# Performance work log

Measured on AMD Instinct MI355X. Metric: run time of the kernel, lower is better.

Reference implementation:

```python
import jax, jax.numpy as jnp
import numpy as np

B, T, DIM = 2, 2048, 2048
N_HEADS, N_KV_HEADS = 32, 8
HEAD_DIM = DIM // N_HEADS          # 64
N_REP = N_HEADS // N_KV_HEADS      # 4
ROPE_THETA = 10000.0


def setup_inputs() -> dict:
    key = jax.random.key(0)
    ks = jax.random.split(key, 5)
    x = jax.random.normal(ks[0], (B, T, DIM), dtype=jnp.float32)
    # RoPE frequencies: freqs_cis[t, j] = exp(i * t * theta^{-2j/head_dim})
    inv_freq = 1.0 / (ROPE_THETA ** (jnp.arange(0, HEAD_DIM, 2, dtype=jnp.float32) / HEAD_DIM))
    angles = jnp.arange(T, dtype=jnp.float32)[:, None] * inv_freq[None, :]  # [T, HEAD_DIM//2]
    cos, sin = jnp.cos(angles), jnp.sin(angles)
    s = 0.02
    wq = jax.random.normal(ks[1], (N_HEADS * HEAD_DIM, DIM), dtype=jnp.float32) * s
    wk = jax.random.normal(ks[2], (N_KV_HEADS * HEAD_DIM, DIM), dtype=jnp.float32) * s
    wv = jax.random.normal(ks[3], (N_KV_HEADS * HEAD_DIM, DIM), dtype=jnp.float32) * s
    wo = jax.random.normal(ks[4], (DIM, DIM), dtype=jnp.float32) * s
    return {"x": x, "cos": cos, "sin": sin, "wq": wq, "wk": wk, "wv": wv, "wo": wo}


def _apply_rope(t, cos, sin):
    # t: [B, T, H, D]; cos/sin: [T, D//2]. Complex multiply on interleaved pairs.
    b, tt, h, d = t.shape
    tr = t.reshape(b, tt, h, d // 2, 2)
    t0, t1 = tr[..., 0], tr[..., 1]
    c = cos[None, :, None, :]
    s = sin[None, :, None, :]
    o0 = t0 * c - t1 * s
    o1 = t0 * s + t1 * c
    return jnp.stack([o0, o1], axis=-1).reshape(b, tt, h, d)


def reference(x, cos, sin, wq, wk, wv, wo):
    Bs, Ts, C = x.shape
    # Projections (nn.Linear, no bias): y = x @ W^T
    q = jnp.einsum('btc,oc->bto', x, wq).reshape(Bs, Ts, N_HEADS, HEAD_DIM)
    k = jnp.einsum('btc,oc->bto', x, wk).reshape(Bs, Ts, N_KV_HEADS, HEAD_DIM)
    v = jnp.einsum('btc,oc->bto', x, wv).reshape(Bs, Ts, N_KV_HEADS, HEAD_DIM)
    q = _apply_rope(q, cos[:Ts], sin[:Ts])
    k = _apply_rope(k, cos[:Ts], sin[:Ts])
    # [B, H, T, D]; GQA: broadcast kv heads via grouped einsum instead of repeat.
    q = q.transpose(0, 2, 1, 3).reshape(Bs, N_KV_HEADS, N_REP, Ts, HEAD_DIM)
    k = k.transpose(0, 2, 1, 3)  # [B, Hkv, T, D]
    v = v.transpose(0, 2, 1, 3)
    scale = 1.0 / jnp.sqrt(jnp.asarray(HEAD_DIM, dtype=x.dtype))
    scores = jnp.einsum('bgrqd,bgkd->bgrqk', q, k) * scale  # [B, Hkv, rep, T, T]
    causal = jnp.tril(jnp.ones((Ts, Ts), dtype=bool))
    scores = jnp.where(causal, scores, jnp.finfo(scores.dtype).min)
    attn = jax.nn.softmax(scores, axis=-1)
    y = jnp.einsum('bgrqk,bgkd->bgrqd', attn, v)           # [B, Hkv, rep, T, D]
    y = y.reshape(Bs, N_HEADS, Ts, HEAD_DIM).transpose(0, 2, 1, 3).reshape(Bs, Ts, C)
    return jnp.einsum('btc,oc->bto', y, wo)
```

## Files before the change

kernel.cpp:

```cpp
#include <hip/hip_runtime.h>

typedef __bf16 bf16;
typedef __attribute__((ext_vector_type(8))) __bf16 bf16x8;
typedef __attribute__((ext_vector_type(4))) __bf16 bf16x4;
typedef __attribute__((ext_vector_type(4))) float f32x4;

constexpr int T_SEQ = 2048;
constexpr int DIM   = 2048;
constexpr int NH    = 32;
constexpr int NKV   = 8;
constexpr int HD    = 64;
constexpr int QKV_N = DIM + 2 * NKV * HD;
constexpr int MROWS = 2 * T_SEQ;

__global__ void cast_all_kernel(const float* __restrict__ x,
                                const float* __restrict__ wq, const float* __restrict__ wk,
                                const float* __restrict__ wv, const float* __restrict__ wo,
                                bf16* __restrict__ xb, bf16* __restrict__ wqkv,
                                bf16* __restrict__ wob) {
  int stride = gridDim.x * blockDim.x;
  for (int g = blockIdx.x * blockDim.x + threadIdx.x; g < 4718592; g += stride) {
    const float* src; bf16* dst; int off;
    if (g < 2097152)      { src = x;  dst = xb;             off = g; }
    else if (g < 3145728) { src = wq; dst = wqkv;           off = g - 2097152; }
    else if (g < 3407872) { src = wk; dst = wqkv + 4194304; off = g - 3145728; }
    else if (g < 3670016) { src = wv; dst = wqkv + 5242880; off = g - 3407872; }
    else                  { src = wo; dst = wob;            off = g - 3670016; }
    float4 v = *(const float4*)(src + (size_t)off * 4);
    bf16x4 o = { (bf16)v.x, (bf16)v.y, (bf16)v.z, (bf16)v.w };
    *(bf16x4*)(dst + (size_t)off * 4) = o;
  }
}

__device__ inline void rect_decode(int orig, int& bmi, int& bni) {
  int c = orig & 7, i = orig >> 3;
  bmi = (c & 1) * 8 + (i & 7);
  bni = (c >> 1) * 4 + (i >> 3);
}

__global__ __launch_bounds__(512) void gemm256(const bf16* __restrict__ A,
                                               const bf16* __restrict__ W,
                                               float* __restrict__ C,
                                               int N, int K) {
  constexpr int BM = 256, BN = 128, BK = 64;
  __shared__ __attribute__((aligned(16))) bf16 Ab[3][BM * BK];
  __shared__ __attribute__((aligned(16))) bf16 Bb[3][BN * BK];
  const int tid = threadIdx.x, lane = tid & 63, wave = tid >> 6;
  const int l15 = lane & 15, l4 = lane >> 4;
  int bmi, bni;
  rect_decode(blockIdx.x, bmi, bni);
  const int bm = bmi * BM, bn = bni * BN;
  const int wm = (wave >> 1) * 64, wn = (wave & 1) * 64;

  f32x4 acc[4][4] = {};

  const int NT = K / BK;
  auto stage = [&](int s, int k0) {
    #pragma unroll
    for (int i = 0; i < 4; ++i) {
      int c = i * 512 + tid;
      int row = c >> 3;
      int gc = ((c & 7) ^ (row & 7)) << 3;
      __builtin_amdgcn_global_load_lds(
          (const __attribute__((address_space(1))) unsigned int*)(A + (size_t)(bm + row) * K + k0 + gc),
          (__attribute__((address_space(3))) unsigned int*)(&Ab[s][0] + c * 8), 16, 0, 0);
    }
    #pragma unroll
    for (int i = 0; i < 2; ++i) {
      int c = i * 512 + tid;
      int row = c >> 3;
      int gc = ((c & 7) ^ (row & 7)) << 3;
      __builtin_amdgcn_global_load_lds(
          (const __attribute__((address_space(1))) unsigned int*)(W + (size_t)(bn + row) * K + k0 + gc),
          (__attribute__((address_space(3))) unsigned int*)(&Bb[s][0] + c * 8), 16, 0, 0);
    }
  };

  stage(0, 0);
  stage(1, BK);

  int d = 0;
  for (int t = 0; t < NT; ++t) {
    if (t + 1 < NT) { asm volatile("s_waitcnt vmcnt(6)" ::: "memory"); }
    else            { asm volatile("s_waitcnt vmcnt(0)" ::: "memory"); }
    __builtin_amdgcn_s_barrier();

    bf16x8 af[2][4], bfr[2][4];
    #pragma unroll
    for (int kk = 0; kk < 2; ++kk) {
      #pragma unroll
      for (int mi = 0; mi < 4; ++mi) {
        int row = wm + mi * 16 + l15;
        af[kk][mi] = *(const bf16x8*)((const char*)&Ab[d][0] + row * 128 +
                                      (((kk * 4 + l4) ^ (row & 7)) << 4));
      }
      #pragma unroll
      for (int ni = 0; ni < 4; ++ni) {
        int row = wn + ni * 16 + l15;
        bfr[kk][ni] = *(const bf16x8*)((const char*)&Bb[d][0] + row * 128 +
                                       (((kk * 4 + l4) ^ (row & 7)) << 4));
      }
    }

    if (t + 2 < NT) {
      int s = d + 2; if (s >= 3) s -= 3;
      stage(s, (t + 2) * BK);
    }

    __builtin_amdgcn_s_setprio(1);
    #pragma unroll
    for (int kk = 0; kk < 2; ++kk)
      #pragma unroll
      for (int mi = 0; mi < 4; ++mi)
        #pragma unroll
        for (int ni = 0; ni < 4; ++ni)
          acc[mi][ni] = __builtin_amdgcn_mfma_f32_16x16x32_bf16(af[kk][mi], bfr[kk][ni],
                                                                acc[mi][ni], 0, 0, 0);
    __builtin_amdgcn_s_setprio(0);

    ++d; if (d == 3) d = 0;
  }

  #pragma unroll
  for (int mi = 0; mi < 4; ++mi)
    #pragma unroll
    for (int ni = 0; ni < 4; ++ni) {
      size_t row = (size_t)bm + wm + mi * 16 + l4 * 4;
      int col = bn + wn + ni * 16 + l15;
      #pragma unroll
      for (int r = 0; r < 4; ++r)
        C[(row + r) * N + col] = acc[mi][ni][r];
    }
}

__global__ __launch_bounds__(512, 1) void gemm192(const bf16* __restrict__ A,
                                                  const bf16* __restrict__ W,
                                                  bf16* __restrict__ C,
                                                  const float* __restrict__ cs,
                                                  const float* __restrict__ sn) {
  constexpr int BM = 256, BN = 192, BK = 64, N = QKV_N, K = DIM;
  __shared__ __attribute__((aligned(16))) bf16 Ab[3][BM * BK];
  __shared__ __attribute__((aligned(16))) bf16 Bb[2][BN * BK];
  const int tid = threadIdx.x, lane = tid & 63, wave = tid >> 6;
  const int l15 = lane & 15, l4 = lane >> 4;
  int bmi, bni;
  rect_decode(blockIdx.x, bmi, bni);
  const int bm = bmi * BM, bn = bni * BN;
  const int wm = (wave >> 1) * 64, wn = (wave & 1) * 96;

  f32x4 acc[4][6] = {};

  constexpr int NT = K / BK;
  auto stageA = [&](int s, int k0) {
    #pragma unroll
    for (int i = 0; i < 4; ++i) {
      int c = i * 512 + tid;
      int row = c >> 3;
      int gc = ((c & 7) ^ (row & 7)) << 3;
      __builtin_amdgcn_global_load_lds(
          (const __attribute__((address_space(1))) unsigned int*)(A + (size_t)(bm + row) * K + k0 + gc),
          (__attribute__((address_space(3))) unsigned int*)(&Ab[s][0] + c * 8), 16, 0, 0);
    }
  };
  auto stageB = [&](int s, int k0) {
    #pragma unroll
    for (int i = 0; i < 3; ++i) {
      int c = i * 512 + tid;
      int row = c >> 3;
      int gc = ((c & 7) ^ (row & 7)) << 3;
      __builtin_amdgcn_global_load_lds(
          (const __attribute__((address_space(1))) unsigned int*)(W + (size_t)(bn + row) * K + k0 + gc),
          (__attribute__((address_space(3))) unsigned int*)(&Bb[s][0] + c * 8), 16, 0, 0);
    }
  };

  stageA(0, 0);
  stageB(0, 0);
  stageA(1, BK);

  for (int t = 0; t < NT; ++t) {
    const int d3 = t % 3, db = t & 1;
    if (t + 1 < NT) { asm volatile("s_waitcnt vmcnt(4)" ::: "memory"); }
    else            { asm volatile("s_waitcnt vmcnt(0)" ::: "memory"); }
    __builtin_amdgcn_s_barrier();

    bf16x8 af[2][4], bfr[2][6];
    #pragma unroll
    for (int kk = 0; kk < 2; ++kk) {
      #pragma unroll
      for (int mi = 0; mi < 4; ++mi) {
        int row = wm + mi * 16 + l15;
        af[kk][mi] = *(const bf16x8*)((const char*)&Ab[d3][0] + row * 128 +
                                      (((kk * 4 + l4) ^ (row & 7)) << 4));
      }
      #pragma unroll
      for (int ni = 0; ni < 6; ++ni) {
        int row = wn + ni * 16 + l15;
        bfr[kk][ni] = *(const bf16x8*)((const char*)&Bb[db][0] + row * 128 +
                                       (((kk * 4 + l4) ^ (row & 7)) << 4));
      }
    }

    if (t + 1 < NT) stageB(db ^ 1, (t + 1) * BK);
    if (t + 2 < NT) { int s = d3 + 2; if (s >= 3) s -= 3; stageA(s, (t + 2) * BK); }

    __builtin_amdgcn_s_setprio(1);
    #pragma unroll
    for (int kk = 0; kk < 2; ++kk)
      #pragma unroll
      for (int mi = 0; mi < 4; ++mi)
        #pragma unroll
        for (int ni = 0; ni < 6; ++ni)
          acc[mi][ni] = __builtin_amdgcn_mfma_f32_16x16x32_bf16(af[kk][mi], bfr[kk][ni],
                                                                acc[mi][ni], 0, 0, 0);
    __builtin_amdgcn_s_setprio(0);
  }

  const bool odd = (l15 & 1);
  #pragma unroll
  for (int ni = 0; ni < 6; ++ni) {
    if (bn + wn + ni * 16 < 2560) {
      int col = bn + wn + ni * 16 + l15;
      int ip = (col & 63) >> 1;
      #pragma unroll
      for (int mi = 0; mi < 4; ++mi) {
        int row0 = wm + mi * 16 + l4 * 4;
        #pragma unroll
        for (int r = 0; r < 4; ++r) {
          int tpos = (bm + row0 + r) & (T_SEQ - 1);
          float c = cs[tpos * 32 + ip];
          float s = sn[tpos * 32 + ip];
          float a = acc[mi][ni][r];
          float p = __shfl_xor(a, 1);
          acc[mi][ni][r] = odd ? (p * s + a * c) : (a * c - p * s);
        }
      }
    }
  }

  #pragma unroll
  for (int mi = 0; mi < 4; ++mi)
    #pragma unroll
    for (int ni = 0; ni < 6; ++ni) {
      size_t row = (size_t)bm + wm + mi * 16 + l4 * 4;
      int col = bn + wn + ni * 16 + l15;
      #pragma unroll
      for (int r = 0; r < 4; ++r)
        C[(row + r) * N + col] = (bf16)acc[mi][ni][r];
    }
}

__global__ __launch_bounds__(512, 2) void attn_kernel(const bf16* __restrict__ qkv,
                                                      bf16* __restrict__ y) {
  const int h = blockIdx.x, b = blockIdx.z;
  const int strip = 15 - blockIdx.y;
  const int g = h >> 2;
  const int tid = threadIdx.x, lane = tid & 63, wave = tid >> 6;
  const int l15 = lane & 15, l4 = lane >> 4;
  const int qbase = strip * 128 + wave * 16;

  __shared__ __attribute__((aligned(16))) bf16 Kb[2][128 * 64];
  __shared__ __attribute__((aligned(16))) bf16 VTs[2][2][64 * 64];
  __shared__ __attribute__((aligned(16))) bf16 Pb[8][16 * 64];

  constexpr float SCALE2 = 0.125f * 1.44269504088896f;
  constexpr float THR_RAW = 8.0f / SCALE2;
  constexpr int VOFF = DIM + NKV * HD;

  const bf16 one1 = (bf16)1.0f;
  const bf16x8 ones = { one1, one1, one1, one1, one1, one1, one1, one1 };

  bf16x8 qf[2];
  {
    const bf16* qp = qkv + ((size_t)b * T_SEQ + qbase + l15) * QKV_N + h * HD + l4 * 8;
    qf[0] = *(const bf16x8*)(qp);
    qf[1] = *(const bf16x8*)(qp + 32);
  }

  f32x4 oacc[4] = {};
  f32x4 lacc = {};
  float m_run = -INFINITY;
  const int qg = qbase + l15;

  const int nt = strip + 1;
  const size_t kvbase = (size_t)b * T_SEQ;
  const int vwoff = ((lane * 128 + wave * 16) ^ ((lane & 7) << 4));

  {
    #pragma unroll
    for (int i = 0; i < 2; ++i) {
      int chunk = i * 512 + tid;
      int row = chunk >> 3;
      int csrc = ((chunk & 7) << 3) ^ ((row & 7) << 3);
      __builtin_amdgcn_global_load_lds(
          (const __attribute__((address_space(1))) unsigned int*)
              (qkv + (kvbase + row) * QKV_N + DIM + g * HD + csrc),
          (__attribute__((address_space(3))) unsigned int*)(&Kb[0][0] + chunk * 8), 16, 0, 0);
    }
    #pragma unroll
    for (int hf = 0; hf < 2; ++hf) {
      const bf16* vp = qkv + (kvbase + hf * 64 + wave * 8) * QKV_N + VOFF + g * HD + lane;
      bf16x8 vr;
      #pragma unroll
      for (int j = 0; j < 8; ++j) vr[j] = vp[(size_t)j * QKV_N];
      *(bf16x8*)((char*)&VTs[0][hf][0] + vwoff) = vr;
    }
    asm volatile("s_waitcnt vmcnt(0)" ::: "memory");
    __syncthreads();
  }

  int cur = 0;
  for (int kt = 0; kt < nt; ++kt) {
    const bool has_next = (kt + 1) < nt;
    bf16x8 vr0, vr1;
    if (has_next) {
      #pragma unroll
      for (int i = 0; i < 2; ++i) {
        int chunk = i * 512 + tid;
        int row = chunk >> 3;
        int csrc = ((chunk & 7) << 3) ^ ((row & 7) << 3);
        __builtin_amdgcn_global_load_lds(
            (const __attribute__((address_space(1))) unsigned int*)
                (qkv + (kvbase + (kt + 1) * 128 + row) * QKV_N + DIM + g * HD + csrc),
            (__attribute__((address_space(3))) unsigned int*)(&Kb[cur ^ 1][0] + chunk * 8), 16, 0, 0);
      }
      const bf16* vp0 = qkv + (kvbase + (kt + 1) * 128 + wave * 8) * QKV_N + VOFF + g * HD + lane;
      const bf16* vp1 = vp0 + (size_t)64 * QKV_N;
      #pragma unroll
      for (int j = 0; j < 8; ++j) vr0[j] = vp0[(size_t)j * QKV_N];
      #pragma unroll
      for (int j = 0; j < 8; ++j) vr1[j] = vp1[(size_t)j * QKV_N];
    }

    const bf16* kb = &Kb[cur][0];
    const bool diag = (kt == strip);

    #pragma unroll
    for (int hf = 0; hf < 2; ++hf) {
      if (diag && hf == 1 && wave < 4) continue;

      f32x4 z[4];
      #pragma unroll
      for (int nt4 = 0; nt4 < 4; ++nt4) z[nt4] = (f32x4){0.f, 0.f, 0.f, 0.f};
      #pragma unroll
      for (int nt4 = 0; nt4 < 4; ++nt4)
        #pragma unroll
        for (int kk = 0; kk < 2; ++kk) {
          bf16x8 kf = *(const bf16x8*)((const char*)kb +
              (((hf * 64 + nt4 * 16 + l15) * 128 + (kk * 32 + l4 * 8) * 2) ^ ((l15 & 7) << 4)));
          z[nt4] = __builtin_amdgcn_mfma_f32_16x16x32_bf16(kf, qf[kk], z[nt4], 0, 0, 0);
        }

      if (diag) {
        #pragma unroll
        for (int nt4 = 0; nt4 < 4; ++nt4)
          #pragma unroll
          for (int r = 0; r < 4; ++r)
            if (kt * 128 + hf * 64 + nt4 * 16 + l4 * 4 + r > qg) z[nt4][r] = -INFINITY;
      }

      float a0 = fmaxf(fmaxf(z[0][0], z[0][1]), z[0][2]);
      float a1 = fmaxf(fmaxf(z[0][3], z[1][0]), z[1][1]);
      float a2 = fmaxf(fmaxf(z[1][2], z[1][3]), z[2][0]);
      float a3 = fmaxf(fmaxf(z[2][1], z[2][2]), z[2][3]);
      float a4 = fmaxf(fmaxf(z[3][0], z[3][1]), z[3][2]);
      float b0 = fmaxf(fmaxf(a0, a1), a2);
      float b1 = fmaxf(fmaxf(a3, a4), z[3][3]);
      float vm = fmaxf(b0, b1);
      vm = fmaxf(vm, __shfl_xor(vm, 16));
      vm = fmaxf(vm, __shfl_xor(vm, 32));

      if (!__all(vm - m_run <= THR_RAW)) {
        float mnew = fmaxf(m_run, vm);
        float alpha = __builtin_amdgcn_exp2f((m_run - mnew) * SCALE2);
        #pragma unroll
        for (int r = 0; r < 4; ++r) lacc[r] *= alpha;
        #pragma unroll
        for (int dt = 0; dt < 4; ++dt)
          #pragma unroll
          for (int r = 0; r < 4; ++r) oacc[dt][r] *= alpha;
        m_run = mnew;
      }
      const float ms = m_run * SCALE2;

      #pragma unroll
      for (int nt4 = 0; nt4 < 4; ++nt4)
        #pragma unroll
        for (int r = 0; r < 4; ++r)
          z[nt4][r] = __builtin_amdgcn_exp2f(__builtin_fmaf(z[nt4][r], SCALE2, -ms));

      bf16* pbw = &Pb[wave][0];
      #pragma unroll
      for (int nt4 = 0; nt4 < 4; ++nt4) {
        bf16x4 pk = { (bf16)z[nt4][0], (bf16)z[nt4][1], (bf16)z[nt4][2], (bf16)z[nt4][3] };
        *(bf16x4*)((char*)pbw + ((l15 * 128 + nt4 * 32 + l4 * 8) ^ ((l15 & 7) << 4))) = pk;
      }

      const bf16* vt = &VTs[cur][hf][0];
      #pragma unroll
      for (int kk = 0; kk < 2; ++kk) {
        bf16x8 pf = *(const bf16x8*)((const char*)pbw +
            ((l15 * 128 + kk * 64 + l4 * 16) ^ ((l15 & 7) << 4)));
        lacc = __builtin_amdgcn_mfma_f32_16x16x32_bf16(ones, pf, lacc, 0, 0, 0);
        #pragma unroll
        for (int dt = 0; dt < 4; ++dt) {
          bf16x8 vf = *(const bf16x8*)((const char*)vt +
              (((dt * 16 + l15) * 128 + (kk * 32 + l4 * 8) * 2) ^ ((l15 & 7) << 4)));
          oacc[dt] = __builtin_amdgcn_mfma_f32_16x16x32_bf16(vf, pf, oacc[dt], 0, 0, 0);
        }
      }
    }

    if (has_next) {
      *(bf16x8*)((char*)&VTs[cur ^ 1][0][0] + vwoff) = vr0;
      *(bf16x8*)((char*)&VTs[cur ^ 1][1][0] + vwoff) = vr1;
      __syncthreads();
      cur ^= 1;
    }
  }

  {
    float linv = __builtin_amdgcn_rcpf(lacc[0]);
    bf16* yp = y + ((size_t)b * T_SEQ + qbase + l15) * DIM + h * HD + l4 * 4;
    #pragma unroll
    for (int dt = 0; dt < 4; ++dt) {
      bf16x4 ov = { (bf16)(oacc[dt][0] * linv), (bf16)(oacc[dt][1] * linv),
                    (bf16)(oacc[dt][2] * linv), (bf16)(oacc[dt][3] * linv) };
      *(bf16x4*)(yp + dt * 16) = ov;
    }
  }
}

extern "C" void kernel_launch(void* const* d_in, const int* in_sizes, int n_in,
                              void* d_out, int out_size, void* d_ws, size_t ws_size,
                              hipStream_t stream) {
  const float* x    = (const float*)d_in[0];
  const float* cosb = (const float*)d_in[1];
  const float* sinb = (const float*)d_in[2];
  const float* wq   = (const float*)d_in[3];
  const float* wk   = (const float*)d_in[4];
  const float* wv   = (const float*)d_in[5];
  const float* wo   = (const float*)d_in[6];
  float* out = (float*)d_out;

  bf16* xb   = (bf16*)d_ws;
  bf16* wqkv = xb + (size_t)MROWS * DIM;
  bf16* wob  = wqkv + (size_t)QKV_N * DIM;
  bf16* qkv  = wob + (size_t)DIM * DIM;
  bf16* y    = qkv + (size_t)MROWS * QKV_N;

  cast_all_kernel<<<2048, 256, 0, stream>>>(x, wq, wk, wv, wo, xb, wqkv, wob);

  gemm192<<<256, 512, 0, stream>>>(xb, wqkv, qkv, cosb, sinb);

  attn_kernel<<<dim3(NH, 16, 2), 512, 0, stream>>>(qkv, y);

  gemm256<<<256, 512, 0, stream>>>(y, wob, out, DIM, DIM);
}
```

Baseline: 164.4 us.

## Process two 256-row query strips per attention block with paired causal balancing

The attention kernel now gives each wave 32 query rows (two 16-row fragments), so every K/V fragment loaded from LDS feeds two MFMAs. Each block handles a long strip (7-p) and a short strip p back-to-back to balance causal work, which shrinks the grid from 1024 to 256 blocks. Launch bounds drop to one block per SM to make room for the doubled accumulators and P buffer. The risks are lower occupancy, fewer blocks than a full wave across the CUs, and some tiles where only part of the waves have causal work to do.

```diff
diff --git a/kernel.cpp b/kernel.cpp
--- a/kernel.cpp
+++ b/kernel.cpp
@@ -250,18 +250,17 @@
     }
 }
 
-__global__ __launch_bounds__(512, 2) void attn_kernel(const bf16* __restrict__ qkv,
+__global__ __launch_bounds__(512, 1) void attn_kernel(const bf16* __restrict__ qkv,
                                                       bf16* __restrict__ y) {
   const int h = blockIdx.x, b = blockIdx.z;
-  const int strip = 15 - blockIdx.y;
+  const int p = blockIdx.y;
   const int g = h >> 2;
   const int tid = threadIdx.x, lane = tid & 63, wave = tid >> 6;
   const int l15 = lane & 15, l4 = lane >> 4;
-  const int qbase = strip * 128 + wave * 16;
 
   __shared__ __attribute__((aligned(16))) bf16 Kb[2][128 * 64];
   __shared__ __attribute__((aligned(16))) bf16 VTs[2][2][64 * 64];
-  __shared__ __attribute__((aligned(16))) bf16 Pb[8][16 * 64];
+  __shared__ __attribute__((aligned(16))) bf16 Pb[8][32 * 64];
 
   constexpr float SCALE2 = 0.125f * 1.44269504088896f;
   constexpr float THR_RAW = 8.0f / SCALE2;
@@ -270,50 +269,31 @@
   const bf16 one1 = (bf16)1.0f;
   const bf16x8 ones = { one1, one1, one1, one1, one1, one1, one1, one1 };
 
-  bf16x8 qf[2];
-  {
-    const bf16* qp = qkv + ((size_t)b * T_SEQ + qbase + l15) * QKV_N + h * HD + l4 * 8;
-    qf[0] = *(const bf16x8*)(qp);
-    qf[1] = *(const bf16x8*)(qp + 32);
-  }
-
-  f32x4 oacc[4] = {};
-  f32x4 lacc = {};
-  float m_run = -INFINITY;
-  const int qg = qbase + l15;
-
-  const int nt = strip + 1;
   const size_t kvbase = (size_t)b * T_SEQ;
   const int vwoff = ((lane * 128 + wave * 16) ^ ((lane & 7) << 4));
 
-  {
-    #pragma unroll
-    for (int i = 0; i < 2; ++i) {
-      int chunk = i * 512 + tid;
-      int row = chunk >> 3;
-      int csrc = ((chunk & 7) << 3) ^ ((row & 7) << 3);
-      __builtin_amdgcn_global_load_lds(
-          (const __attribute__((address_space(1))) unsigned int*)
-              (qkv + (kvbase + row) * QKV_N + DIM + g * HD + csrc),
-          (__attribute__((address_space(3))) unsigned int*)(&Kb[0][0] + chunk * 8), 16, 0, 0);
-    }
-    #pragma unroll
-    for (int hf = 0; hf < 2; ++hf) {
-      const bf16* vp = qkv + (kvbase + hf * 64 + wave * 8) * QKV_N + VOFF + g * HD + lane;
-      bf16x8 vr;
-      #pragma unroll
-      for (int j = 0; j < 8; ++j) vr[j] = vp[(size_t)j * QKV_N];
-      *(bf16x8*)((char*)&VTs[0][hf][0] + vwoff) = vr;
-    }
-    asm volatile("s_waitcnt vmcnt(0)" ::: "memory");
+  #pragma unroll
+  for (int sp = 0; sp < 2; ++sp) {
+    const int strip = sp == 0 ? (7 - p) : p;
+    const int qbase = strip * 256 + wave * 32;
+    const int last_kt = (qbase + 31) >> 7;
+    const int nt = 2 * strip + 2;
+
     __syncthreads();
-  }
-
-  int cur = 0;
-  for (int kt = 0; kt < nt; ++kt) {
-    const bool has_next = (kt + 1) < nt;
-    bf16x8 vr0, vr1;
-    if (has_next) {
+
+    bf16x8 qf[2][2];
+    #pragma unroll
+    for (int f = 0; f < 2; ++f) {
+      const bf16* qp = qkv + ((size_t)b * T_SEQ + qbase + f * 16 + l15) * QKV_N + h * HD + l4 * 8;
+      qf[f][0] = *(const bf16x8*)(qp);
+      qf[f][1] = *(const bf16x8*)(qp + 32);
+    }
+
+    f32x4 oacc[2][4] = {};
+    f32x4 lacc[2] = {};
+    float m_run[2] = {-INFINITY, -INFINITY};
+
+    {
       #pragma unroll
       for (int i = 0; i < 2; ++i) {
         int chunk = i * 512 + tid;
@@ -321,112 +301,156 @@
         int csrc = ((chunk & 7) << 3) ^ ((row & 7) << 3);
         __builtin_amdgcn_global_load_lds(
             (const __attribute__((address_space(1))) unsigned int*)
-                (qkv + (kvbase + (kt + 1) * 128 + row) * QKV_N + DIM + g * HD + csrc),
-            (__attribute__((address_space(3))) unsigned int*)(&Kb[cur ^ 1][0] + chunk * 8), 16, 0, 0);
-      }
-      const bf16* vp0 = qkv + (kvbase + (kt + 1) * 128 + wave * 8) * QKV_N + VOFF + g * HD + lane;
-      const bf16* vp1 = vp0 + (size_t)64 * QKV_N;
-      #pragma unroll
-      for (int j = 0; j < 8; ++j) vr0[j] = vp0[(size_t)j * QKV_N];
-      #pragma unroll
-      for (int j = 0; j < 8; ++j) vr1[j] = vp1[(size_t)j * QKV_N];
-    }
-
-    const bf16* kb = &Kb[cur][0];
-    const bool diag = (kt == strip);
-
-    #pragma unroll
-    for (int hf = 0; hf < 2; ++hf) {
-      if (diag && hf == 1 && wave < 4) continue;
-
-      f32x4 z[4];
-      #pragma unroll
-      for (int nt4 = 0; nt4 < 4; ++nt4) z[nt4] = (f32x4){0.f, 0.f, 0.f, 0.f};
-      #pragma unroll
-      for (int nt4 = 0; nt4 < 4; ++nt4)
-        #pragma unroll
-        for (int kk = 0; kk < 2; ++kk) {
-          bf16x8 kf = *(const bf16x8*)((const char*)kb +
-              (((hf * 64 + nt4 * 16 + l15) * 128 + (kk * 32 + l4 * 8) * 2) ^ ((l15 & 7) << 4)));
-          z[nt4] = __builtin_amdgcn_mfma_f32_16x16x32_bf16(kf, qf[kk], z[nt4], 0, 0, 0);
+                (qkv + (kvbase + row) * QKV_N + DIM + g * HD + csrc),
+            (__attribute__((address_space(3))) unsigned int*)(&Kb[0][0] + chunk * 8), 16, 0, 0);
+      }
+      #pragma unroll
+      for (int hf = 0; hf < 2; ++hf) {
+        const bf16* vp = qkv + (kvbase + hf * 64 + wave * 8) * QKV_N + VOFF + g * HD + lane;
+        bf16x8 vr;
+        #pragma unroll
+        for (int j = 0; j < 8; ++j) vr[j] = vp[(size_t)j * QKV_N];
+        *(bf16x8*)((char*)&VTs[0][hf][0] + vwoff) = vr;
+      }
+      asm volatile("s_waitcnt vmcnt(0)" ::: "memory");
+      __syncthreads();
+    }
+
+    int cur = 0;
+    for (int kt = 0; kt < nt; ++kt) {
+      const bool has_next = (kt + 1) < nt;
+      bf16x8 vr0, vr1;
+      if (has_next) {
+        #pragma unroll
+        for (int i = 0; i < 2; ++i) {
+          int chunk = i * 512 + tid;
+          int row = chunk >> 3;
+          int csrc = ((chunk & 7) << 3) ^ ((row & 7) << 3);
+          __builtin_amdgcn_global_load_lds(
+              (const __attribute__((address_space(1))) unsigned int*)
+                  (qkv + (kvbase + (kt + 1) * 128 + row) * QKV_N + DIM + g * HD + csrc),
+              (__attribute__((address_space(3))) unsigned int*)(&Kb[cur ^ 1][0] + chunk * 8), 16, 0, 0);
         }
-
-      if (diag) {
-        #pragma unroll
-        for (int nt4 = 0; nt4 < 4; ++nt4)
+        const bf16* vp0 = qkv + (kvbase + (kt + 1) * 128 + wave * 8) * QKV_N + VOFF + g * HD + lane;
+        const bf16* vp1 = vp0 + (size_t)64 * QKV_N;
+        #pragma unroll
+        for (int j = 0; j < 8; ++j) vr0[j] = vp0[(size_t)j * QKV_N];
+        #pragma unroll
+        for (int j = 0; j < 8; ++j) vr1[j] = vp1[(size_t)j * QKV_N];
+      }
+
+      if (kt <= last_kt) {
+        const bf16* kb = &Kb[cur][0];
+        const bool diag = (kt == last_kt);
+
+        #pragma unroll
+        for (int hf = 0; hf < 2; ++hf) {
+          if (diag && (kt * 128 + hf * 64 > qbase + 31)) continue;
+
+          f32x4 z[2][4];
           #pragma unroll
-          for (int r = 0; r < 4; ++r)
-            if (kt * 128 + hf * 64 + nt4 * 16 + l4 * 4 + r > qg) z[nt4][r] = -INFINITY;
-      }
-
-      float a0 = fmaxf(fmaxf(z[0][0], z[0][1]), z[0][2]);
-      float a1 = fmaxf(fmaxf(z[0][3], z[1][0]), z[1][1]);
-      float a2 = fmaxf(fmaxf(z[1][2], z[1][3]), z[2][0]);
-      float a3 = fmaxf(fmaxf(z[2][1], z[2][2]), z[2][3]);
-      float a4 = fmaxf(fmaxf(z[3][0], z[3][1]), z[3][2]);
-      float b0 = fmaxf(fmaxf(a0, a1), a2);
-      float b1 = fmaxf(fmaxf(a3, a4), z[3][3]);
-      float vm = fmaxf(b0, b1);
-      vm = fmaxf(vm, __shfl_xor(vm, 16));
-      vm = fmaxf(vm, __shfl_xor(vm, 32));
-
-      if (!__all(vm - m_run <= THR_RAW)) {
-        float mnew = fmaxf(m_run, vm);
-        float alpha = __builtin_amdgcn_exp2f((m_run - mnew) * SCALE2);
-        #pragma unroll
-        for (int r = 0; r < 4; ++r) lacc[r] *= alpha;
-        #pragma unroll
-        for (int dt = 0; dt < 4; ++dt)
+          for (int f = 0; f < 2; ++f)
+            #pragma unroll
+            for (int nt4 = 0; nt4 < 4; ++nt4) z[f][nt4] = (f32x4){0.f, 0.f, 0.f, 0.f};
           #pragma unroll
-          for (int r = 0; r < 4; ++r) oacc[dt][r] *= alpha;
-        m_run = mnew;
-      }
-      const float ms = m_run * SCALE2;
-
-      #pragma unroll
-      for (int nt4 = 0; nt4 < 4; ++nt4)
-        #pragma unroll
-        for (int r = 0; r < 4; ++r)
-          z[nt4][r] = __builtin_amdgcn_exp2f(__builtin_fmaf(z[nt4][r], SCALE2, -ms));
-
-      bf16* pbw = &Pb[wave][0];
-      #pragma unroll
-      for (int nt4 = 0; nt4 < 4; ++nt4) {
-        bf16x4 pk = { (bf16)z[nt4][0], (bf16)z[nt4][1], (bf16)z[nt4][2], (bf16)z[nt4][3] };
-        *(bf16x4*)((char*)pbw + ((l15 * 128 + nt4 * 32 + l4 * 8) ^ ((l15 & 7) << 4))) = pk;
-      }
-
-      const bf16* vt = &VTs[cur][hf][0];
-      #pragma unroll
-      for (int kk = 0; kk < 2; ++kk) {
-        bf16x8 pf = *(const bf16x8*)((const char*)pbw +
-            ((l15 * 128 + kk * 64 + l4 * 16) ^ ((l15 & 7) << 4)));
-        lacc = __builtin_amdgcn_mfma_f32_16x16x32_bf16(ones, pf, lacc, 0, 0, 0);
-        #pragma unroll
-        for (int dt = 0; dt < 4; ++dt) {
-          bf16x8 vf = *(const bf16x8*)((const char*)vt +
-              (((dt * 16 + l15) * 128 + (kk * 32 + l4 * 8) * 2) ^ ((l15 & 7) << 4)));
-          oacc[dt] = __builtin_amdgcn_mfma_f32_16x16x32_bf16(vf, pf, oacc[dt], 0, 0, 0);
+          for (int nt4 = 0; nt4 < 4; ++nt4)
+            #pragma unroll
+            for (int kk = 0; kk < 2; ++kk) {
+              bf16x8 kf = *(const bf16x8*)((const char*)kb +
+                  (((hf * 64 + nt4 * 16 + l15) * 128 + (kk * 32 + l4 * 8) * 2) ^ ((l15 & 7) << 4)));
+              z[0][nt4] = __builtin_amdgcn_mfma_f32_16x16x32_bf16(kf, qf[0][kk], z[0][nt4], 0, 0, 0);
+              z[1][nt4] = __builtin_amdgcn_mfma_f32_16x16x32_bf16(kf, qf[1][kk], z[1][nt4], 0, 0, 0);
+            }
+
+          bf16* pbw = &Pb[wave][0];
+          #pragma unroll
+          for (int f = 0; f < 2; ++f) {
+            const int qg = qbase + f * 16 + l15;
+            if (diag) {
+              #pragma unroll
+              for (int nt4 = 0; nt4 < 4; ++nt4)
+                #pragma unroll
+                for (int r = 0; r < 4; ++r)
+                  if (kt * 128 + hf * 64 + nt4 * 16 + l4 * 4 + r > qg) z[f][nt4][r] = -INFINITY;
+            }
+
+            float a0 = fmaxf(fmaxf(z[f][0][0], z[f][0][1]), z[f][0][2]);
+            float a1 = fmaxf(fmaxf(z[f][0][3], z[f][1][0]), z[f][1][1]);
+            float a2 = fmaxf(fmaxf(z[f][1][2], z[f][1][3]), z[f][2][0]);
+            float a3 = fmaxf(fmaxf(z[f][2][1], z[f][2][2]), z[f][2][3]);
+            float a4 = fmaxf(fmaxf(z[f][3][0], z[f][3][1]), z[f][3][2]);
+            float b0 = fmaxf(fmaxf(a0, a1), a2);
+            float b1 = fmaxf(fmaxf(a3, a4), z[f][3][3]);
+            float vm = fmaxf(b0, b1);
+            vm = fmaxf(vm, __shfl_xor(vm, 16));
+            vm = fmaxf(vm, __shfl_xor(vm, 32));
+
+            if (!__all(vm - m_run[f] <= THR_RAW)) {
+              float mnew = fmaxf(m_run[f], vm);
+              float alpha = __builtin_amdgcn_exp2f((m_run[f] - mnew) * SCALE2);
+              #pragma unroll
+              for (int r = 0; r < 4; ++r) lacc[f][r] *= alpha;
+              #pragma unroll
+              for (int dt = 0; dt < 4; ++dt)
+                #pragma unroll
+                for (int r = 0; r < 4; ++r) oacc[f][dt][r] *= alpha;
+              m_run[f] = mnew;
+            }
+            const float ms = m_run[f] * SCALE2;
+
+            #pragma unroll
+            for (int nt4 = 0; nt4 < 4; ++nt4)
+              #pragma unroll
+              for (int r = 0; r < 4; ++r)
+                z[f][nt4][r] = __builtin_amdgcn_exp2f(__builtin_fmaf(z[f][nt4][r], SCALE2, -ms));
+
+            const int row = f * 16 + l15;
+            #pragma unroll
+            for (int nt4 = 0; nt4 < 4; ++nt4) {
+              bf16x4 pk = { (bf16)z[f][nt4][0], (bf16)z[f][nt4][1],
+                            (bf16)z[f][nt4][2], (bf16)z[f][nt4][3] };
+              *(bf16x4*)((char*)pbw + ((row * 128 + nt4 * 32 + l4 * 8) ^ ((row & 7) << 4))) = pk;
+            }
+          }
+
+          const bf16* vt = &VTs[cur][hf][0];
+          #pragma unroll
+          for (int kk = 0; kk < 2; ++kk) {
+            bf16x8 pf0 = *(const bf16x8*)((const char*)pbw +
+                ((l15 * 128 + kk * 64 + l4 * 16) ^ ((l15 & 7) << 4)));
+            bf16x8 pf1 = *(const bf16x8*)((const char*)pbw +
+                (((16 + l15) * 128 + kk * 64 + l4 * 16) ^ ((l15 & 7) << 4)));
+            lacc[0] = __builtin_amdgcn_mfma_f32_16x16x32_bf16(ones, pf0, lacc[0], 0, 0, 0);
+            lacc[1] = __builtin_amdgcn_mfma_f32_16x16x32_bf16(ones, pf1, lacc[1], 0, 0, 0);
+            #pragma unroll
+            for (int dt = 0; dt < 4; ++dt) {
+              bf16x8 vf = *(const bf16x8*)((const char*)vt +
+                  (((dt * 16 + l15) * 128 + (kk * 32 + l4 * 8) * 2) ^ ((l15 & 7) << 4)));
+              oacc[0][dt] = __builtin_amdgcn_mfma_f32_16x16x32_bf16(vf, pf0, oacc[0][dt], 0, 0, 0);
+              oacc[1][dt] = __builtin_amdgcn_mfma_f32_16x16x32_bf16(vf, pf1, oacc[1][dt], 0, 0, 0);
+            }
+          }
         }
       }
-    }
-
-    if (has_next) {
-      *(bf16x8*)((char*)&VTs[cur ^ 1][0][0] + vwoff) = vr0;
-      *(bf16x8*)((char*)&VTs[cur ^ 1][1][0] + vwoff) = vr1;
-      __syncthreads();
-      cur ^= 1;
-    }
-  }
-
-  {
-    float linv = __builtin_amdgcn_rcpf(lacc[0]);
-    bf16* yp = y + ((size_t)b * T_SEQ + qbase + l15) * DIM + h * HD + l4 * 4;
-    #pragma unroll
-    for (int dt = 0; dt < 4; ++dt) {
-      bf16x4 ov = { (bf16)(oacc[dt][0] * linv), (bf16)(oacc[dt][1] * linv),
-                    (bf16)(oacc[dt][2] * linv), (bf16)(oacc[dt][3] * linv) };
-      *(bf16x4*)(yp + dt * 16) = ov;
+
+      if (has_next) {
+        *(bf16x8*)((char*)&VTs[cur ^ 1][0][0] + vwoff) = vr0;
+        *(bf16x8*)((char*)&VTs[cur ^ 1][1][0] + vwoff) = vr1;
+        __syncthreads();
+        cur ^= 1;
+      }
+    }
+
+    #pragma unroll
+    for (int f = 0; f < 2; ++f) {
+      float linv = __builtin_amdgcn_rcpf(lacc[f][0]);
+      bf16* yp = y + ((size_t)b * T_SEQ + qbase + f * 16 + l15) * DIM + h * HD + l4 * 4;
+      #pragma unroll
+      for (int dt = 0; dt < 4; ++dt) {
+        bf16x4 ov = { (bf16)(oacc[f][dt][0] * linv), (bf16)(oacc[f][dt][1] * linv),
+                      (bf16)(oacc[f][dt][2] * linv), (bf16)(oacc[f][dt][3] * linv) };
+        *(bf16x4*)(yp + dt * 16) = ov;
+      }
     }
   }
 }
@@ -453,7 +477,7 @@
 
   gemm192<<<256, 512, 0, stream>>>(xb, wqkv, qkv, cosb, sinb);
 
-  attn_kernel<<<dim3(NH, 16, 2), 512, 0, stream>>>(qkv, y);
+  attn_kernel<<<dim3(NH, 4, 2), 512, 0, stream>>>(qkv, y);
 
   gemm256<<<256, 512, 0, stream>>>(y, wob, out, DIM, DIM);
 }
```

After: 173.8 us. +5.7%, slower.

## Single-buffer K/V LDS tiles in attention to allow three blocks per CU

Applied to the files above, without the earlier changes.

Drops the LDS double buffers for K and V^T in the attention kernel. Next-tile K is now loaded into registers, no longer through asynchronous global-to-LDS copies, and stored to LDS between two barriers after compute finishes. Launch bounds are raised to three 512-thread blocks per CU. The aim is higher occupancy through a smaller LDS footprint, at the cost of an extra barrier per tile, more registers per thread and less overlap between loads and compute.

```diff
diff --git a/kernel.cpp b/kernel.cpp
--- a/kernel.cpp
+++ b/kernel.cpp
@@ -250,7 +250,7 @@
     }
 }
 
-__global__ __launch_bounds__(512, 2) void attn_kernel(const bf16* __restrict__ qkv,
+__global__ __launch_bounds__(512, 3) void attn_kernel(const bf16* __restrict__ qkv,
                                                       bf16* __restrict__ y) {
   const int h = blockIdx.x, b = blockIdx.z;
   const int strip = 15 - blockIdx.y;
@@ -259,8 +259,8 @@
   const int l15 = lane & 15, l4 = lane >> 4;
   const int qbase = strip * 128 + wave * 16;
 
-  __shared__ __attribute__((aligned(16))) bf16 Kb[2][128 * 64];
-  __shared__ __attribute__((aligned(16))) bf16 VTs[2][2][64 * 64];
+  __shared__ __attribute__((aligned(16))) bf16 Kb[128 * 64];
+  __shared__ __attribute__((aligned(16))) bf16 VTs[2][64 * 64];
   __shared__ __attribute__((aligned(16))) bf16 Pb[8][16 * 64];
 
   constexpr float SCALE2 = 0.125f * 1.44269504088896f;
@@ -285,6 +285,7 @@
   const int nt = strip + 1;
   const size_t kvbase = (size_t)b * T_SEQ;
   const int vwoff = ((lane * 128 + wave * 16) ^ ((lane & 7) << 4));
+  const int krow = tid >> 2, kcb = tid & 3;
 
   {
     #pragma unroll
@@ -295,7 +296,7 @@
       __builtin_amdgcn_global_load_lds(
           (const __attribute__((address_space(1))) unsigned int*)
               (qkv + (kvbase + row) * QKV_N + DIM + g * HD + csrc),
-          (__attribute__((address_space(3))) unsigned int*)(&Kb[0][0] + chunk * 8), 16, 0, 0);
+          (__attribute__((address_space(3))) unsigned int*)(&Kb[0] + chunk * 8), 16, 0, 0);
     }
     #pragma unroll
     for (int hf = 0; hf < 2; ++hf) {
@@ -303,26 +304,21 @@
       bf16x8 vr;
       #pragma unroll
       for (int j = 0; j < 8; ++j) vr[j] = vp[(size_t)j * QKV_N];
-      *(bf16x8*)((char*)&VTs[0][hf][0] + vwoff) = vr;
+      *(bf16x8*)((char*)&VTs[hf][0] + vwoff) = vr;
     }
     asm volatile("s_waitcnt vmcnt(0)" ::: "memory");
     __syncthreads();
   }
 
-  int cur = 0;
   for (int kt = 0; kt < nt; ++kt) {
     const bool has_next = (kt + 1) < nt;
-    bf16x8 vr0, vr1;
+    bf16x8 kr0, kr1, vr0, vr1;
     if (has_next) {
-      #pragma unroll
-      for (int i = 0; i < 2; ++i) {
-        int chunk = i * 512 + tid;
-        int row = chunk >> 3;
-        int csrc = ((chunk & 7) << 3) ^ ((row & 7) << 3);
-        __builtin_amdgcn_global_load_lds(
-            (const __attribute__((address_space(1))) unsigned int*)
-                (qkv + (kvbase + (kt + 1) * 128 + row) * QKV_N + DIM + g * HD + csrc),
-            (__attribute__((address_space(3))) unsigned int*)(&Kb[cur ^ 1][0] + chunk * 8), 16, 0, 0);
+      {
+        int c0 = tid, c1 = 512 + tid;
+        int r0 = c0 >> 3, r1 = c1 >> 3;
+        kr0 = *(const bf16x8*)(qkv + (kvbase + (kt + 1) * 128 + r0) * QKV_N + DIM + g * HD + (c0 & 7) * 8);
+        kr1 = *(const bf16x8*)(qkv + (kvbase + (kt + 1) * 128 + r1) * QKV_N + DIM + g * HD + (c1 & 7) * 8);
       }
       const bf16* vp0 = qkv + (kvbase + (kt + 1) * 128 + wave * 8) * QKV_N + VOFF + g * HD + lane;
       const bf16* vp1 = vp0 + (size_t)64 * QKV_N;
@@ -332,7 +328,6 @@
       for (int j = 0; j < 8; ++j) vr1[j] = vp1[(size_t)j * QKV_N];
     }
 
-    const bf16* kb = &Kb[cur][0];
     const bool diag = (kt == strip);
 
     #pragma unroll
@@ -346,7 +341,7 @@
       for (int nt4 = 0; nt4 < 4; ++nt4)
         #pragma unroll
         for (int kk = 0; kk < 2; ++kk) {
-          bf16x8 kf = *(const bf16x8*)((const char*)kb +
+          bf16x8 kf = *(const bf16x8*)((const char*)&Kb[0] +
               (((hf * 64 + nt4 * 16 + l15) * 128 + (kk * 32 + l4 * 8) * 2) ^ ((l15 & 7) << 4)));
           z[nt4] = __builtin_amdgcn_mfma_f32_16x16x32_bf16(kf, qf[kk], z[nt4], 0, 0, 0);
         }
@@ -396,7 +391,7 @@
         *(bf16x4*)((char*)pbw + ((l15 * 128 + nt4 * 32 + l4 * 8) ^ ((l15 & 7) << 4))) = pk;
       }
 
-      const bf16* vt = &VTs[cur][hf][0];
+      const bf16* vt = &VTs[hf][0];
       #pragma unroll
       for (int kk = 0; kk < 2; ++kk) {
         bf16x8 pf = *(const bf16x8*)((const char*)pbw +
@@ -412,10 +407,16 @@
     }
 
     if (has_next) {
-      *(bf16x8*)((char*)&VTs[cur ^ 1][0][0] + vwoff) = vr0;
-      *(bf16x8*)((char*)&VTs[cur ^ 1][1][0] + vwoff) = vr1;
       __syncthreads();
-      cur ^= 1;
+      {
+        int c0 = tid, c1 = 512 + tid;
+        int r0 = c0 >> 3, r1 = c1 >> 3;
+        *(bf16x8*)((char*)&Kb[0] + r0 * 128 + (((c0 & 7) ^ (r0 & 7)) << 4)) = kr0;
+        *(bf16x8*)((char*)&Kb[0] + r1 * 128 + (((c1 & 7) ^ (r1 & 7)) << 4)) = kr1;
+      }
+      *(bf16x8*)((char*)&VTs[0][0] + vwoff) = vr0;
+      *(bf16x8*)((char*)&VTs[1][0] + vwoff) = vr1;
+      __syncthreads();
     }
   }
 
```

Measured after the change: 187.7 us. 14.2% more time.
